# Kernel tuning notes

Measured on AMD Instinct MI355X. Metric: run time of the kernel, lower is better.

Reference implementation:

```python
import jax, jax.numpy as jnp
import numpy as np


def setup_inputs() -> dict:
    key = jax.random.key(0)
    k1, k2, k3, k4, k5 = jax.random.split(key, 5)
    B, T, D, H = 256, 2048, 128, 128
    s = 1.0 / np.sqrt(H)  # torch LSTMCell default init scale
    return {
        "x": jax.random.normal(k1, (B, T, D), dtype=jnp.float32),
        "W_ih": jax.random.normal(k2, (4 * H, D), dtype=jnp.float32) * s,
        "W_hh": jax.random.normal(k3, (4 * H, H), dtype=jnp.float32) * s,
        "b_ih": jax.random.normal(k4, (4 * H,), dtype=jnp.float32) * s,
        "b_hh": jax.random.normal(k5, (4 * H,), dtype=jnp.float32) * s,
    }


def _att_lstm(x, W_ih, W_hh, b_ih, b_hh):
    B, T, D = x.shape
    H = W_hh.shape[1]
    # Precompute input projections for all timesteps in one big GEMM.
    x_proj = jnp.einsum('btd,gd->btg', x, W_ih) + b_ih  # [B, T, 4H]

    def step(carry, xp_t):
        h, c = carry
        gates = xp_t + h @ W_hh.T + b_hh  # [B, 4H]
        i, f, g, o = jnp.split(gates, 4, axis=-1)  # torch gate order i,f,g,o
        c = jax.nn.sigmoid(f) * c + jax.nn.sigmoid(i) * jnp.tanh(g)
        h = jax.nn.sigmoid(o) * jnp.tanh(c)
        return (h, c), h

    h0 = jnp.zeros((B, H), dtype=x.dtype)
    (h_last, _), h_states = jax.lax.scan(step, (h0, h0), jnp.swapaxes(x_proj, 0, 1))
    h_states = jnp.swapaxes(h_states, 0, 1)  # [B, T, H]

    # Dot-product attention pooling against the final hidden state.
    att_score = jnp.einsum('bth,bh->bt', h_states, h_last)  # [B, T]
    att_dist = jax.nn.softmax(att_score, axis=1)
    return jnp.einsum('bt,bth->bh', att_dist, h_states)  # [B, H]


def reference(x, W_ih, W_hh, b_ih, b_hh):
    return _att_lstm(x, W_ih, W_hh, b_ih, b_hh)
```

## Files before the change

### kernel.cpp

```cpp
#include <hip/hip_runtime.h>
#include <math.h>

#define B_ 256
#define T_ 2048
#define D_ 128
#define H_ 128
#define CHUNK 16
#define NCHUNK (T_ / CHUNK)
#define XPITCH 136

typedef _Float16 f16;
typedef __attribute__((ext_vector_type(8))) _Float16 f16x8;
typedef __attribute__((ext_vector_type(4))) _Float16 f16x4;
typedef __attribute__((ext_vector_type(2))) _Float16 f16x2;
typedef __attribute__((ext_vector_type(4))) float f32x4;

__device__ __forceinline__ float sigf(float x) { return 1.0f / (1.0f + __expf(-x)); }
__device__ __forceinline__ float tanh_fast(float x) {
    return 1.0f - 2.0f / (1.0f + __expf(2.0f * x));
}

__global__ __launch_bounds__(512, 2)
void lstm_scan(const float* __restrict__ x,
               const float* __restrict__ W_ih,
               const float* __restrict__ W_hh,
               const float* __restrict__ b_ih,
               const float* __restrict__ b_hh,
               float* __restrict__ h_states) {
    const int b   = blockIdx.x;
    const int tid = threadIdx.x;
    const int w   = tid >> 6;
    const int l   = tid & 63;
    const int l15 = l & 15;
    const int lg  = l >> 4;
    const int jw  = (w << 4) | l15;

    __shared__ __align__(16) f16   h2[2][H_];
    __shared__ __align__(16) f16   x_lds[CHUNK][XPITCH];
    __shared__ __align__(16) float proj_lds[CHUNK][H_][4];

    f16x8 wbh[4][4];
    f16x8 wbi[4][4];
    float bias[4];
    #pragma unroll
    for (int q = 0; q < 4; q++) {
        const int g = q * H_ + jw;
        bias[q] = b_ih[g] + b_hh[g];
        #pragma unroll
        for (int kk = 0; kk < 4; kk++) {
            const float* ph = W_hh + (size_t)g * H_ + kk * 32 + lg * 8;
            const float* pi = W_ih + (size_t)g * D_ + kk * 32 + lg * 8;
            f16x8 vh, vi;
            #pragma unroll
            for (int e = 0; e < 8; e++) { vh[e] = (f16)ph[e]; vi[e] = (f16)pi[e]; }
            wbh[q][kk] = vh; wbi[q][kk] = vi;
        }
    }

    if (tid < 64) ((unsigned int*)&h2[0][0])[tid] = 0u;

    const float* xb = x + (size_t)b * T_ * D_;
    float* hs = h_states + (size_t)b * T_ * H_;

    float4 xpre = ((const float4*)xb)[tid];

    float cst = 0.0f;
    float h_prev = 0.0f;

    for (int c = 0; c < NCHUNK; c++) {
        {
            const int ts = tid >> 5;
            const int d0 = (tid & 31) * 4;
            f16x4 pk;
            pk[0] = (f16)xpre.x; pk[1] = (f16)xpre.y;
            pk[2] = (f16)xpre.z; pk[3] = (f16)xpre.w;
            *(f16x4*)&x_lds[ts][d0] = pk;
        }
        __syncthreads();

        if (c + 1 < NCHUNK)
            xpre = ((const float4*)(xb + (size_t)(c + 1) * CHUNK * D_))[tid];

        f32x4 pacc[4] = {{0,0,0,0},{0,0,0,0},{0,0,0,0},{0,0,0,0}};
        {
            f16x8 ax[4];
            #pragma unroll
            for (int kk = 0; kk < 4; kk++)
                ax[kk] = *(const f16x8*)&x_lds[l15][kk * 32 + lg * 8];
            #pragma unroll
            for (int q = 0; q < 4; q++)
                #pragma unroll
                for (int kk = 0; kk < 4; kk++)
                    pacc[q] = __builtin_amdgcn_mfma_f32_16x16x32_f16(
                        ax[kk], wbi[q][kk], pacc[q], 0, 0, 0);
        }
        #pragma unroll
        for (int r = 0; r < 4; r++) {
            f32x4 row = { pacc[0][r], pacc[1][r], pacc[2][r], pacc[3][r] };
            *(f32x4*)&proj_lds[lg * 4 + r][jw][0] = row;
        }
        __syncthreads();

        #pragma unroll 4
        for (int tt = 0; tt < CHUNK; tt++) {
            const int t = c * CHUNK + tt;
            if (t > 0 && lg == 0) hs[(size_t)(t - 1) * H_ + jw] = h_prev;

            const f32x4 seed4 = *(const f32x4*)&proj_lds[tt][jw][0];

            f16x8 ah[4];
            const f16* hb = h2[tt & 1];
            #pragma unroll
            for (int kk = 0; kk < 4; kk++)
                ah[kk] = *(const f16x8*)&hb[kk * 32 + lg * 8];

            f32x4 acc[4];
            #pragma unroll
            for (int q = 0; q < 4; q++) {
                const float s = seed4[q] + bias[q];
                f32x4 cc = { s, s, s, s };
                #pragma unroll
                for (int kk = 0; kk < 4; kk++)
                    cc = __builtin_amdgcn_mfma_f32_16x16x32_f16(
                        ah[kk], wbh[q][kk], cc, 0, 0, 0);
                acc[q] = cc;
            }
            const float ig = sigf(acc[0][0]);
            const float fg = sigf(acc[1][0]);
            const float gt = tanh_fast(acc[2][0]);
            const float og = sigf(acc[3][0]);
            cst = fg * cst + ig * gt;
            const float h = og * tanh_fast(cst);
            h_prev = h;

            const float hn = __shfl_xor(h, 1);
            if (lg == 0 && (l15 & 1) == 0) {
                f16x2 pr; pr[0] = (f16)h; pr[1] = (f16)hn;
                *(f16x2*)&h2[(tt + 1) & 1][jw] = pr;
            }
            __syncthreads();
        }
    }
    if (lg == 0) hs[(size_t)(T_ - 1) * H_ + jw] = h_prev;
}

__global__ __launch_bounds__(512)
void attention(const float* __restrict__ h_states,
               float* __restrict__ out) {
    const int b   = blockIdx.x;
    const int tid = threadIdx.x;

    __shared__ float h_lds[H_];
    __shared__ float sc[T_];
    __shared__ float red[16];
    __shared__ float part[4][H_];

    const float* hs = h_states + (size_t)b * T_ * H_;
    if (tid < H_) h_lds[tid] = hs[(size_t)(T_ - 1) * H_ + tid];
    __syncthreads();

    const float4* hl4 = (const float4*)h_lds;
    #pragma unroll 1
    for (int q = 0; q < 4; q++) {
        const int t = q * 512 + tid;
        const float4* hr = (const float4*)(hs + (size_t)t * H_);
        float a0 = 0.f, a1 = 0.f, a2 = 0.f, a3 = 0.f;
        #pragma unroll
        for (int i = 0; i < H_ / 16; i++) {
            float4 r0 = hr[i*4+0], l0 = hl4[i*4+0];
            float4 r1 = hr[i*4+1], l1 = hl4[i*4+1];
            float4 r2 = hr[i*4+2], l2 = hl4[i*4+2];
            float4 r3 = hr[i*4+3], l3 = hl4[i*4+3];
            a0 += r0.x*l0.x + r0.y*l0.y + r0.z*l0.z + r0.w*l0.w;
            a1 += r1.x*l1.x + r1.y*l1.y + r1.z*l1.z + r1.w*l1.w;
            a2 += r2.x*l2.x + r2.y*l2.y + r2.z*l2.z + r2.w*l2.w;
            a3 += r3.x*l3.x + r3.y*l3.y + r3.z*l3.z + r3.w*l3.w;
        }
        sc[t] = (a0 + a1) + (a2 + a3);
    }

    float m = -3.0e38f;
    #pragma unroll
    for (int q = 0; q < 4; q++) m = fmaxf(m, sc[q * 512 + tid]);
    #pragma unroll
    for (int off = 1; off < 64; off <<= 1) m = fmaxf(m, __shfl_xor(m, off));
    if ((tid & 63) == 0) red[tid >> 6] = m;
    __syncthreads();
    float mx = red[0];
    #pragma unroll
    for (int w2 = 1; w2 < 8; w2++) mx = fmaxf(mx, red[w2]);

    float ssum = 0.f;
    #pragma unroll
    for (int q = 0; q < 4; q++) {
        float e = __expf(sc[q * 512 + tid] - mx);
        sc[q * 512 + tid] = e;
        ssum += e;
    }
    #pragma unroll
    for (int off = 1; off < 64; off <<= 1) ssum += __shfl_xor(ssum, off);
    if ((tid & 63) == 0) red[8 + (tid >> 6)] = ssum;
    __syncthreads();
    float tot = 0.f;
    #pragma unroll
    for (int w2 = 0; w2 < 8; w2++) tot += red[8 + w2];
    const float inv = 1.0f / tot;

    {
        const int j = tid & 127;
        const int q = tid >> 7;
        const float* hp  = hs + (size_t)q * 512 * H_ + j;
        const float* scp = sc + q * 512;
        float a0 = 0.f, a1 = 0.f, a2 = 0.f, a3 = 0.f;
        #pragma unroll 4
        for (int t = 0; t < 512; t += 4) {
            a0 += scp[t+0] * hp[(size_t)(t+0) * H_];
            a1 += scp[t+1] * hp[(size_t)(t+1) * H_];
            a2 += scp[t+2] * hp[(size_t)(t+2) * H_];
            a3 += scp[t+3] * hp[(size_t)(t+3) * H_];
        }
        part[q][j] = (a0 + a1) + (a2 + a3);
    }
    __syncthreads();
    if (tid < H_) {
        out[(size_t)b * H_ + tid] =
            (part[0][tid] + part[1][tid] + part[2][tid] + part[3][tid]) * inv;
    }
}

extern "C" void kernel_launch(void* const* d_in, const int* in_sizes, int n_in,
                              void* d_out, int out_size, void* d_ws, size_t ws_size,
                              hipStream_t stream) {
    const float* x    = (const float*)d_in[0];
    const float* W_ih = (const float*)d_in[1];
    const float* W_hh = (const float*)d_in[2];
    const float* b_ih = (const float*)d_in[3];
    const float* b_hh = (const float*)d_in[4];
    float* out = (float*)d_out;

    float* h_states = (float*)d_ws;

    lstm_scan<<<B_, 512, 0, stream>>>(x, W_ih, W_hh, b_ih, b_hh, h_states);
    attention<<<B_, 512, 0, stream>>>(h_states, out);
}
```

Measured before the change: 1.814 ms.

## Store hidden states in fp16, prepack weights, and split MFMA accumulation chains

Adds a pack_weights kernel that converts W_ih and W_hh to fp16 in the MFMA register layout. The scan reloads W_ih fragments each chunk instead of keeping them resident, which lowers register pressure. Hidden states are staged in LDS and written to global as fp16 with coalesced per-chunk stores, which halves h_states traffic for the attention kernel. The recurrent MFMA chain is split into two independent accumulators to shorten the dependency latency, bias is folded into the projection, and the attention kernel is adapted to read fp16 with an 8-way time split. Storing hidden states in fp16 lowers the precision of the attention inputs, and the extra pack launch adds a small fixed cost.

```diff
diff --git a/kernel.cpp b/kernel.cpp
--- a/kernel.cpp
+++ b/kernel.cpp
@@ -14,19 +14,40 @@
 typedef __attribute__((ext_vector_type(4))) _Float16 f16x4;
 typedef __attribute__((ext_vector_type(2))) _Float16 f16x2;
 typedef __attribute__((ext_vector_type(4))) float f32x4;
+typedef __attribute__((ext_vector_type(2))) float f32x2;
 
 __device__ __forceinline__ float sigf(float x) { return 1.0f / (1.0f + __expf(-x)); }
 __device__ __forceinline__ float tanh_fast(float x) {
     return 1.0f - 2.0f / (1.0f + __expf(2.0f * x));
 }
 
+__global__ void pack_weights(const float* __restrict__ W_ih,
+                             const float* __restrict__ W_hh,
+                             f16* __restrict__ pih, f16* __restrict__ phh) {
+    const int idx = blockIdx.x * 256 + threadIdx.x;
+    const int m = idx >> 13;
+    const int r = idx & 8191;
+    const int w  = r >> 10;
+    const int q  = (r >> 8) & 3;
+    const int kk = (r >> 6) & 3;
+    const int l  = r & 63;
+    const int g  = q * 128 + w * 16 + (l & 15);
+    const int k0 = kk * 32 + (l >> 4) * 8;
+    const float* src = (m ? W_hh : W_ih) + (size_t)g * 128 + k0;
+    f16* dst = (m ? phh : pih) + (size_t)r * 8;
+    f16x8 v;
+    #pragma unroll
+    for (int e = 0; e < 8; e++) v[e] = (f16)src[e];
+    *(f16x8*)dst = v;
+}
+
 __global__ __launch_bounds__(512, 2)
 void lstm_scan(const float* __restrict__ x,
-               const float* __restrict__ W_ih,
-               const float* __restrict__ W_hh,
+               const f16* __restrict__ pih,
+               const f16* __restrict__ phh,
                const float* __restrict__ b_ih,
                const float* __restrict__ b_hh,
-               float* __restrict__ h_states) {
+               f16* __restrict__ h_states) {
     const int b   = blockIdx.x;
     const int tid = threadIdx.x;
     const int w   = tid >> 6;
@@ -37,37 +58,44 @@
 
     __shared__ __align__(16) f16   h2[2][H_];
     __shared__ __align__(16) f16   x_lds[CHUNK][XPITCH];
+    __shared__ __align__(16) f16   hbuf[CHUNK][H_];
     __shared__ __align__(16) float proj_lds[CHUNK][H_][4];
 
     f16x8 wbh[4][4];
-    f16x8 wbi[4][4];
+    {
+        const f16x8* ph = (const f16x8*)phh;
+        #pragma unroll
+        for (int q = 0; q < 4; q++)
+            #pragma unroll
+            for (int kk = 0; kk < 4; kk++)
+                wbh[q][kk] = ph[(w * 16 + q * 4 + kk) * 64 + l];
+    }
     float bias[4];
     #pragma unroll
-    for (int q = 0; q < 4; q++) {
-        const int g = q * H_ + jw;
-        bias[q] = b_ih[g] + b_hh[g];
-        #pragma unroll
-        for (int kk = 0; kk < 4; kk++) {
-            const float* ph = W_hh + (size_t)g * H_ + kk * 32 + lg * 8;
-            const float* pi = W_ih + (size_t)g * D_ + kk * 32 + lg * 8;
-            f16x8 vh, vi;
-            #pragma unroll
-            for (int e = 0; e < 8; e++) { vh[e] = (f16)ph[e]; vi[e] = (f16)pi[e]; }
-            wbh[q][kk] = vh; wbi[q][kk] = vi;
-        }
-    }
+    for (int q = 0; q < 4; q++) bias[q] = b_ih[q * 128 + jw] + b_hh[q * 128 + jw];
 
     if (tid < 64) ((unsigned int*)&h2[0][0])[tid] = 0u;
 
     const float* xb = x + (size_t)b * T_ * D_;
-    float* hs = h_states + (size_t)b * T_ * H_;
+    f16* hs = h_states + (size_t)b * T_ * H_;
 
     float4 xpre = ((const float4*)xb)[tid];
-
     float cst = 0.0f;
-    float h_prev = 0.0f;
 
     for (int c = 0; c < NCHUNK; c++) {
+        f16x8 wbi[4][4];
+        {
+            const f16x8* pi = (const f16x8*)pih;
+            #pragma unroll
+            for (int q = 0; q < 4; q++)
+                #pragma unroll
+                for (int kk = 0; kk < 4; kk++)
+                    wbi[q][kk] = pi[(w * 16 + q * 4 + kk) * 64 + l];
+        }
+
+        f16x4 hb;
+        if (c > 0) hb = ((const f16x4*)hbuf)[tid];
+
         {
             const int ts = tid >> 5;
             const int d0 = (tid & 31) * 4;
@@ -78,74 +106,78 @@
         }
         __syncthreads();
 
+        if (c > 0)
+            *(f16x4*)(hs + (size_t)(c - 1) * CHUNK * H_ + (size_t)tid * 4) = hb;
+
         if (c + 1 < NCHUNK)
             xpre = ((const float4*)(xb + (size_t)(c + 1) * CHUNK * D_))[tid];
 
-        f32x4 pacc[4] = {{0,0,0,0},{0,0,0,0},{0,0,0,0},{0,0,0,0}};
         {
             f16x8 ax[4];
             #pragma unroll
             for (int kk = 0; kk < 4; kk++)
                 ax[kk] = *(const f16x8*)&x_lds[l15][kk * 32 + lg * 8];
+            f32x4 pacc[4] = {{0,0,0,0},{0,0,0,0},{0,0,0,0},{0,0,0,0}};
             #pragma unroll
             for (int q = 0; q < 4; q++)
                 #pragma unroll
                 for (int kk = 0; kk < 4; kk++)
                     pacc[q] = __builtin_amdgcn_mfma_f32_16x16x32_f16(
                         ax[kk], wbi[q][kk], pacc[q], 0, 0, 0);
-        }
-        #pragma unroll
-        for (int r = 0; r < 4; r++) {
-            f32x4 row = { pacc[0][r], pacc[1][r], pacc[2][r], pacc[3][r] };
-            *(f32x4*)&proj_lds[lg * 4 + r][jw][0] = row;
+            #pragma unroll
+            for (int r = 0; r < 4; r++) {
+                f32x4 row = { pacc[0][r] + bias[0], pacc[1][r] + bias[1],
+                              pacc[2][r] + bias[2], pacc[3][r] + bias[3] };
+                *(f32x4*)&proj_lds[lg * 4 + r][jw][0] = row;
+            }
         }
         __syncthreads();
 
-        #pragma unroll 4
+        #pragma unroll 8
         for (int tt = 0; tt < CHUNK; tt++) {
-            const int t = c * CHUNK + tt;
-            if (t > 0 && lg == 0) hs[(size_t)(t - 1) * H_ + jw] = h_prev;
-
             const f32x4 seed4 = *(const f32x4*)&proj_lds[tt][jw][0];
 
             f16x8 ah[4];
-            const f16* hb = h2[tt & 1];
+            const f16* hb2 = h2[tt & 1];
             #pragma unroll
             for (int kk = 0; kk < 4; kk++)
-                ah[kk] = *(const f16x8*)&hb[kk * 32 + lg * 8];
-
-            f32x4 acc[4];
+                ah[kk] = *(const f16x8*)&hb2[kk * 32 + lg * 8];
+
+            float gate[4];
             #pragma unroll
             for (int q = 0; q < 4; q++) {
-                const float s = seed4[q] + bias[q];
-                f32x4 cc = { s, s, s, s };
-                #pragma unroll
-                for (int kk = 0; kk < 4; kk++)
-                    cc = __builtin_amdgcn_mfma_f32_16x16x32_f16(
-                        ah[kk], wbh[q][kk], cc, 0, 0, 0);
-                acc[q] = cc;
+                f32x4 ca = { seed4[q], 0.f, 0.f, 0.f };
+                ca = __builtin_amdgcn_mfma_f32_16x16x32_f16(ah[0], wbh[q][0], ca, 0, 0, 0);
+                ca = __builtin_amdgcn_mfma_f32_16x16x32_f16(ah[1], wbh[q][1], ca, 0, 0, 0);
+                f32x4 cb = { 0.f, 0.f, 0.f, 0.f };
+                cb = __builtin_amdgcn_mfma_f32_16x16x32_f16(ah[2], wbh[q][2], cb, 0, 0, 0);
+                cb = __builtin_amdgcn_mfma_f32_16x16x32_f16(ah[3], wbh[q][3], cb, 0, 0, 0);
+                gate[q] = ca[0] + cb[0];
             }
-            const float ig = sigf(acc[0][0]);
-            const float fg = sigf(acc[1][0]);
-            const float gt = tanh_fast(acc[2][0]);
-            const float og = sigf(acc[3][0]);
+
+            const float ig = sigf(gate[0]);
+            const float fg = sigf(gate[1]);
+            const float gt = tanh_fast(gate[2]);
+            const float og = sigf(gate[3]);
             cst = fg * cst + ig * gt;
             const float h = og * tanh_fast(cst);
-            h_prev = h;
-
-            const float hn = __shfl_xor(h, 1);
-            if (lg == 0 && (l15 & 1) == 0) {
-                f16x2 pr; pr[0] = (f16)h; pr[1] = (f16)hn;
-                *(f16x2*)&h2[(tt + 1) & 1][jw] = pr;
+
+            if (lg == 0) {
+                const f16 hf = (f16)h;
+                h2[(tt + 1) & 1][jw] = hf;
+                hbuf[tt][jw] = hf;
             }
             __syncthreads();
         }
     }
-    if (lg == 0) hs[(size_t)(T_ - 1) * H_ + jw] = h_prev;
+    {
+        f16x4 hb = ((const f16x4*)hbuf)[tid];
+        *(f16x4*)(hs + (size_t)(NCHUNK - 1) * CHUNK * H_ + (size_t)tid * 4) = hb;
+    }
 }
 
 __global__ __launch_bounds__(512)
-void attention(const float* __restrict__ h_states,
+void attention(const f16* __restrict__ h_states,
                float* __restrict__ out) {
     const int b   = blockIdx.x;
     const int tid = threadIdx.x;
@@ -153,31 +185,28 @@
     __shared__ float h_lds[H_];
     __shared__ float sc[T_];
     __shared__ float red[16];
-    __shared__ float part[4][H_];
-
-    const float* hs = h_states + (size_t)b * T_ * H_;
-    if (tid < H_) h_lds[tid] = hs[(size_t)(T_ - 1) * H_ + tid];
-    __syncthreads();
-
-    const float4* hl4 = (const float4*)h_lds;
+    __shared__ float part[8][H_];
+
+    const f16* hs = h_states + (size_t)b * T_ * H_;
+    if (tid < H_) h_lds[tid] = (float)hs[(size_t)(T_ - 1) * H_ + tid];
+    __syncthreads();
+
     #pragma unroll 1
     for (int q = 0; q < 4; q++) {
         const int t = q * 512 + tid;
-        const float4* hr = (const float4*)(hs + (size_t)t * H_);
-        float a0 = 0.f, a1 = 0.f, a2 = 0.f, a3 = 0.f;
+        const f16x8* hr = (const f16x8*)(hs + (size_t)t * H_);
+        float a0 = 0.f, a1 = 0.f;
         #pragma unroll
-        for (int i = 0; i < H_ / 16; i++) {
-            float4 r0 = hr[i*4+0], l0 = hl4[i*4+0];
-            float4 r1 = hr[i*4+1], l1 = hl4[i*4+1];
-            float4 r2 = hr[i*4+2], l2 = hl4[i*4+2];
-            float4 r3 = hr[i*4+3], l3 = hl4[i*4+3];
-            a0 += r0.x*l0.x + r0.y*l0.y + r0.z*l0.z + r0.w*l0.w;
-            a1 += r1.x*l1.x + r1.y*l1.y + r1.z*l1.z + r1.w*l1.w;
-            a2 += r2.x*l2.x + r2.y*l2.y + r2.z*l2.z + r2.w*l2.w;
-            a3 += r3.x*l3.x + r3.y*l3.y + r3.z*l3.z + r3.w*l3.w;
-        }
-        sc[t] = (a0 + a1) + (a2 + a3);
-    }
+        for (int i = 0; i < 16; i++) {
+            f16x8 v = hr[i];
+            a0 += (float)v[0] * h_lds[i*8+0] + (float)v[1] * h_lds[i*8+1]
+                + (float)v[2] * h_lds[i*8+2] + (float)v[3] * h_lds[i*8+3];
+            a1 += (float)v[4] * h_lds[i*8+4] + (float)v[5] * h_lds[i*8+5]
+                + (float)v[6] * h_lds[i*8+6] + (float)v[7] * h_lds[i*8+7];
+        }
+        sc[t] = a0 + a1;
+    }
+    __syncthreads();
 
     float m = -3.0e38f;
     #pragma unroll
@@ -207,24 +236,26 @@
     const float inv = 1.0f / tot;
 
     {
-        const int j = tid & 127;
-        const int q = tid >> 7;
-        const float* hp  = hs + (size_t)q * 512 * H_ + j;
-        const float* scp = sc + q * 512;
-        float a0 = 0.f, a1 = 0.f, a2 = 0.f, a3 = 0.f;
+        const int j2 = (tid & 63) * 2;
+        const int qq = tid >> 6;
+        const f16* base = hs + (size_t)qq * 256 * H_ + j2;
+        const float* scp = sc + qq * 256;
+        float a0 = 0.f, a1 = 0.f;
         #pragma unroll 4
-        for (int t = 0; t < 512; t += 4) {
-            a0 += scp[t+0] * hp[(size_t)(t+0) * H_];
-            a1 += scp[t+1] * hp[(size_t)(t+1) * H_];
-            a2 += scp[t+2] * hp[(size_t)(t+2) * H_];
-            a3 += scp[t+3] * hp[(size_t)(t+3) * H_];
-        }
-        part[q][j] = (a0 + a1) + (a2 + a3);
+        for (int t = 0; t < 256; t++) {
+            f16x2 v = *(const f16x2*)(base + (size_t)t * H_);
+            const float wgt = scp[t];
+            a0 += wgt * (float)v[0];
+            a1 += wgt * (float)v[1];
+        }
+        *(f32x2*)&part[qq][j2] = (f32x2){ a0, a1 };
     }
     __syncthreads();
     if (tid < H_) {
-        out[(size_t)b * H_ + tid] =
-            (part[0][tid] + part[1][tid] + part[2][tid] + part[3][tid]) * inv;
+        float s = 0.f;
+        #pragma unroll
+        for (int qq = 0; qq < 8; qq++) s += part[qq][tid];
+        out[(size_t)b * H_ + tid] = s * inv;
     }
 }
 
@@ -238,8 +269,11 @@
     const float* b_hh = (const float*)d_in[4];
     float* out = (float*)d_out;
 
-    float* h_states = (float*)d_ws;
-
-    lstm_scan<<<B_, 512, 0, stream>>>(x, W_ih, W_hh, b_ih, b_hh, h_states);
-    attention<<<B_, 512, 0, stream>>>(h_states, out);
-}
+    f16* hs16 = (f16*)d_ws;
+    f16* pih  = (f16*)((char*)d_ws + (size_t)B_ * T_ * H_ * 2);
+    f16* phh  = pih + 8192 * 8;
+
+    pack_weights<<<64, 256, 0, stream>>>(W_ih, W_hh, pih, phh);
+    lstm_scan<<<B_, 512, 0, stream>>>(x, pih, phh, b_ih, b_hh, hs16);
+    attention<<<B_, 512, 0, stream>>>(hs16, out);
+}
```

After: 1.705 ms. 6.0% less time.
